# Performance work log

Measured on AMD Instinct MI355X. Metric: run time of the kernel, lower is better.

Reference implementation:

```python
import jax, jax.numpy as jnp
import numpy as np

BS, C_IN, SEQ_LEN = 16, 321, 720
PRED_LEN, PATCH_LEN, STRIDE = 720, 24, 24
N_LAYERS, D_MODEL, N_HEADS, D_FF = 3, 128, 16, 256
SEQ_PN = (SEQ_LEN - PATCH_LEN) // STRIDE + 1   # 30
PRED_PN = (PRED_LEN + PATCH_LEN - 1) // PATCH_LEN  # 30
EPS = 1e-5


def layernorm(x, g, b):
    mu = x.mean(-1, keepdims=True)
    var = x.var(-1, keepdims=True)
    return (x - mu) * jax.lax.rsqrt(var + EPS) * g + b


def setup_inputs() -> dict:
    key = jax.random.key(0)
    ks = iter(jax.random.split(key, 32))
    w = lambda shape, s=0.02: jax.random.normal(next(ks), shape, jnp.float32) * s
    L = N_LAYERS
    return {
        "z": jax.random.normal(next(ks), (BS, C_IN, SEQ_LEN), jnp.float32),
        "W_P_w": w((D_MODEL, PATCH_LEN)), "W_P_b": jnp.zeros((D_MODEL,), jnp.float32),
        "PE": 0.04 * jax.random.uniform(next(ks), (SEQ_PN, D_MODEL), jnp.float32) - 0.02,
        "dummies": 0.5 * jax.random.normal(next(ks), (C_IN, PRED_PN, PATCH_LEN), jnp.float32),
        "Wq": w((L, D_MODEL, D_MODEL)), "bq": jnp.zeros((L, D_MODEL), jnp.float32),
        "Wk": w((L, D_MODEL, D_MODEL)), "bk": jnp.zeros((L, D_MODEL), jnp.float32),
        "Wv": w((L, D_MODEL, D_MODEL)), "bv": jnp.zeros((L, D_MODEL), jnp.float32),
        "Wo": w((L, D_MODEL, D_MODEL)), "bo": jnp.zeros((L, D_MODEL), jnp.float32),
        "g1": jnp.ones((L, D_MODEL), jnp.float32), "be1": jnp.zeros((L, D_MODEL), jnp.float32),
        "W1": w((L, D_FF, D_MODEL)), "b1": jnp.zeros((L, D_FF), jnp.float32),
        "W2": w((L, D_MODEL, D_FF // 2)), "b2": jnp.zeros((L, D_MODEL), jnp.float32),
        "g2": jnp.ones((L, D_MODEL), jnp.float32), "be2": jnp.zeros((L, D_MODEL), jnp.float32),
        "proj_w": w((PATCH_LEN, D_MODEL)), "proj_b": jnp.zeros((PATCH_LEN,), jnp.float32),
    }


def reference(z, W_P_w, W_P_b, PE, dummies, Wq, bq, Wk, bk, Wv, bv, Wo, bo,
              g1, be1, W1, b1, W2, b2, g2, be2, proj_w, proj_b):
    bs, c, _ = z.shape
    d_h = D_MODEL // N_HEADS
    scale = d_h ** -0.5
    # instance norm over time (unbiased=False var)
    mean = z.mean(2, keepdims=True)
    std = jnp.sqrt(z.var(2, keepdims=True) + EPS)
    zn = (z - mean) / std
    # unfold into patches: [bs, c, S, patch_len]
    idx = jnp.arange(SEQ_PN)[:, None] * STRIDE + jnp.arange(PATCH_LEN)[None, :]
    patches = zn[:, :, idx]
    x = jnp.einsum('bcsp,dp->bcsd', patches, W_P_w) + W_P_b + PE
    x = x.reshape(bs * c, SEQ_PN, D_MODEL)                       # seq tokens
    dum = jnp.einsum('cnp,dp->cnd', dummies, W_P_w) + W_P_b      # [c, Pn, d]
    pred = jnp.broadcast_to(dum[None], (bs, c, PRED_PN, D_MODEL)).reshape(bs * c, PRED_PN, D_MODEL)
    B = bs * c
    scores = None
    for i in range(N_LAYERS):
        q = (jnp.einsum('bpd,ed->bpe', pred, Wq[i]) + bq[i]).reshape(B, PRED_PN, N_HEADS, d_h)
        k = (jnp.einsum('bsd,ed->bse', x, Wk[i]) + bk[i]).reshape(B, SEQ_PN, N_HEADS, d_h)
        v = (jnp.einsum('bsd,ed->bse', x, Wv[i]) + bv[i]).reshape(B, SEQ_PN, N_HEADS, d_h)
        s = jnp.einsum('bphd,bshd->bphs', q, k) * scale
        if scores is not None:
            s = s + scores   # residual attention scores across layers
        scores = s
        attn = jax.nn.softmax(s, axis=-1)
        o = jnp.einsum('bphs,bshd->bphd', attn, v).reshape(B, PRED_PN, D_MODEL)
        o = jnp.einsum('bpd,ed->bpe', o, Wo[i]) + bo[i]
        pred = layernorm(pred + o, g1[i], be1[i])
        h = jnp.einsum('bpd,fd->bpf', pred, W1[i]) + b1[i]
        a, gate = jnp.split(h, 2, axis=-1)
        f = jnp.einsum('bpf,df->bpd', a * jax.nn.gelu(gate, approximate=False), W2[i]) + b2[i]
        pred = layernorm(pred + f, g2[i], be2[i])
    out = pred.reshape(bs, c, PRED_PN, D_MODEL)
    out = jnp.einsum('bcnd,pd->bcnp', out, proj_w) + proj_b
    out = out.reshape(bs, c, PRED_PN * PATCH_LEN)
    return out * std[:, :, 0:1] + mean[:, :, 0:1]
```

## Files before the change

kernel.cpp:

```cpp
#include <hip/hip_runtime.h>
#include <math.h>


typedef unsigned short u16;
typedef __attribute__((ext_vector_type(8))) short short8;
typedef __attribute__((ext_vector_type(4))) float floatx4;

#define ATTN_SCALE 0.35355339059327373f
#define SB 136
#define BUFSZ (30*SB)

#define MFMA_BF16 __builtin_amdgcn_mfma_f32_16x16x32_bf16

__device__ __forceinline__ u16 f2bf(float f){
  union{ __bf16 b; u16 u; } v; v.b = (__bf16)f;
  return v.u;
}
__device__ __forceinline__ float bf2f(u16 h){
  union{unsigned u; float f;} v; v.u = ((unsigned)h)<<16;
  return v.f;
}
__device__ __forceinline__ unsigned pk2bf(float lo, float hi){
  union{ __bf16 b[2]; unsigned u; } v;
  v.b[0] = (__bf16)lo; v.b[1] = (__bf16)hi;
  return v.u;
}
__device__ __forceinline__ float dot2bf(unsigned a, unsigned b, float c){
  float d;
  asm("v_dot2_f32_bf16 %0, %1, %2, %3" : "=v"(d) : "v"(a), "v"(b), "v"(c));
  return d;
}
__device__ __forceinline__ float gelu_f(float x){
  float u = x*(1.f + 0.044715f*x*x);
  float e = __expf(-1.5957691216057308f*u);
  return x/(1.f+e);
}

__device__ __forceinline__ short8 cvt8(const float* ap){
  floatx4 f0 = *(const floatx4*)ap;
  floatx4 f1 = *(const floatx4*)(ap+4);
  short8 a;
  a[0]=(short)f2bf(f0[0]); a[1]=(short)f2bf(f0[1]);
  a[2]=(short)f2bf(f0[2]); a[3]=(short)f2bf(f0[3]);
  a[4]=(short)f2bf(f1[0]); a[5]=(short)f2bf(f1[1]);
  a[6]=(short)f2bf(f1[2]); a[7]=(short)f2bf(f1[3]);
  return a;
}
__device__ __forceinline__ short8 loadB(const u16* p){ return *(const short8*)p; }
__device__ __forceinline__ short8 loadB(const float* p){ return cvt8(p); }

__device__ __forceinline__ void epi(u16* out, floatx4 acc, float bv, float oscale,
                                    int rt, int qd, int col){
  #pragma unroll
  for (int r=0;r<4;++r){
    const int row = rt*16+qd*4+r;
    if (row<30) out[row*SB+col] = f2bf((acc[r]+bv)*oscale);
  }
}

template<typename WT>
__device__ __forceinline__ void gemm2(const u16* A, const WT* __restrict__ W,
                                      const float* __restrict__ bias, u16* out,
                                      int wave, int lane, float oscale){
  const int m=lane&15, qd=lane>>4, c0=wave*16+m;
  floatx4 acc[2][2] = {{{0.f,0.f,0.f,0.f},{0.f,0.f,0.f,0.f}},
                       {{0.f,0.f,0.f,0.f},{0.f,0.f,0.f,0.f}}};
  #pragma unroll
  for (int kt=0;kt<4;++kt){
    short8 b0 = loadB(W + c0*128       + kt*32 + qd*8);
    short8 b1 = loadB(W + (c0+64)*128  + kt*32 + qd*8);
    #pragma unroll
    for (int rt=0;rt<2;++rt){
      short8 a = *(const short8*)(A + (rt*16+m)*SB + kt*32 + qd*8);
      acc[0][rt] = MFMA_BF16(a, b0, acc[0][rt], 0,0,0);
      acc[1][rt] = MFMA_BF16(a, b1, acc[1][rt], 0,0,0);
    }
  }
  #pragma unroll
  for (int ct=0;ct<2;++ct){
    const int col = c0 + ct*64;
    const float bv = bias[col];
    #pragma unroll
    for (int rt=0;rt<2;++rt) epi(out, acc[ct][rt], bv, oscale, rt, qd, col);
  }
}

template<typename WT>
__device__ __forceinline__ void gemm_kv(const u16* A,
                                        const WT* __restrict__ Wk, const float* __restrict__ bk,
                                        const WT* __restrict__ Wv, const float* __restrict__ bv_,
                                        u16* outk, u16* outv, int wave, int lane){
  const int m=lane&15, qd=lane>>4, c0=wave*16+m;
  floatx4 acck[2][2] = {{{0.f,0.f,0.f,0.f},{0.f,0.f,0.f,0.f}},
                        {{0.f,0.f,0.f,0.f},{0.f,0.f,0.f,0.f}}};
  floatx4 accv[2][2] = {{{0.f,0.f,0.f,0.f},{0.f,0.f,0.f,0.f}},
                        {{0.f,0.f,0.f,0.f},{0.f,0.f,0.f,0.f}}};
  #pragma unroll
  for (int kt=0;kt<4;++kt){
    short8 bk0 = loadB(Wk + c0*128      + kt*32 + qd*8);
    short8 bk1 = loadB(Wk + (c0+64)*128 + kt*32 + qd*8);
    short8 bv0 = loadB(Wv + c0*128      + kt*32 + qd*8);
    short8 bv1 = loadB(Wv + (c0+64)*128 + kt*32 + qd*8);
    #pragma unroll
    for (int rt=0;rt<2;++rt){
      short8 a = *(const short8*)(A + (rt*16+m)*SB + kt*32 + qd*8);
      acck[0][rt] = MFMA_BF16(a, bk0, acck[0][rt], 0,0,0);
      acck[1][rt] = MFMA_BF16(a, bk1, acck[1][rt], 0,0,0);
      accv[0][rt] = MFMA_BF16(a, bv0, accv[0][rt], 0,0,0);
      accv[1][rt] = MFMA_BF16(a, bv1, accv[1][rt], 0,0,0);
    }
  }
  #pragma unroll
  for (int ct=0;ct<2;++ct){
    const int col = c0 + ct*64;
    const float bkb = bk[col], bvb = bv_[col];
    #pragma unroll
    for (int rt=0;rt<2;++rt){
      epi(outk, acck[ct][rt], bkb, 1.f, rt, qd, col);
      epi(outv, accv[ct][rt], bvb, 1.f, rt, qd, col);
    }
  }
}

template<typename WT>
__device__ __forceinline__ void gemm_h(const u16* A, const WT* __restrict__ W1,
                                       const float* __restrict__ b1, u16* out,
                                       int wave, int lane){
  const int m=lane&15, qd=lane>>4, c0=wave*16+m;
  floatx4 acca[2][2] = {{{0.f,0.f,0.f,0.f},{0.f,0.f,0.f,0.f}},
                        {{0.f,0.f,0.f,0.f},{0.f,0.f,0.f,0.f}}};
  floatx4 accg[2][2] = {{{0.f,0.f,0.f,0.f},{0.f,0.f,0.f,0.f}},
                        {{0.f,0.f,0.f,0.f},{0.f,0.f,0.f,0.f}}};
  #pragma unroll
  for (int kt=0;kt<4;++kt){
    short8 ba0 = loadB(W1 + c0*128        + kt*32 + qd*8);
    short8 ba1 = loadB(W1 + (c0+64)*128   + kt*32 + qd*8);
    short8 bg0 = loadB(W1 + (c0+128)*128  + kt*32 + qd*8);
    short8 bg1 = loadB(W1 + (c0+192)*128  + kt*32 + qd*8);
    #pragma unroll
    for (int rt=0;rt<2;++rt){
      short8 a = *(const short8*)(A + (rt*16+m)*SB + kt*32 + qd*8);
      acca[0][rt] = MFMA_BF16(a, ba0, acca[0][rt], 0,0,0);
      acca[1][rt] = MFMA_BF16(a, ba1, acca[1][rt], 0,0,0);
      accg[0][rt] = MFMA_BF16(a, bg0, accg[0][rt], 0,0,0);
      accg[1][rt] = MFMA_BF16(a, bg1, accg[1][rt], 0,0,0);
    }
  }
  #pragma unroll
  for (int ct=0;ct<2;++ct){
    const int ca = c0 + ct*64;
    const float bab = b1[ca], bgb = b1[128+ca];
    #pragma unroll
    for (int rt=0;rt<2;++rt){
      #pragma unroll
      for (int r=0;r<4;++r){
        const int row = rt*16+qd*4+r;
        if (row<30){
          float a = acca[ct][rt][r]+bab;
          float g = accg[ct][rt][r]+bgb;
          out[row*SB+ca] = f2bf(a * gelu_f(g));
        }
      }
    }
  }
}

__device__ __forceinline__ void ln_res_reg(float (&p0)[8], float (&p1)[8],
                                           const u16* add, u16* predb,
                                           const float* __restrict__ g, const float* __restrict__ be,
                                           int wave, int lane){
  #pragma unroll
  for (int idx=0; idx<8; ++idx){
    const int row = wave + idx*4;
    if (row < 30){
      float v0 = p0[idx] + bf2f(add[row*SB+lane]);
      float v1 = p1[idx] + bf2f(add[row*SB+lane+64]);
      float s = v0+v1, s2 = v0*v0+v1*v1;
      #pragma unroll
      for (int off=32; off>0; off>>=1){ s += __shfl_xor(s,off,64); s2 += __shfl_xor(s2,off,64); }
      float m = s*(1.f/128.f);
      float var = s2*(1.f/128.f) - m*m;
      float rstd = rsqrtf(var + 1e-5f);
      float o0 = (v0-m)*rstd*g[lane]    + be[lane];
      float o1 = (v1-m)*rstd*g[lane+64] + be[lane+64];
      p0[idx] = o0; p1[idx] = o1;
      predb[row*SB+lane]    = f2bf(o0);
      predb[row*SB+lane+64] = f2bf(o1);
    }
  }
}

__global__ void cvtw(const float* __restrict__ Wq, const float* __restrict__ Wk,
                     const float* __restrict__ Wv, const float* __restrict__ Wo,
                     const float* __restrict__ W1, const float* __restrict__ W2,
                     u16* __restrict__ ws){
  const int i = blockIdx.x*256 + threadIdx.x;
  float v;
  if      (i < 49152)  v = Wq[i];
  else if (i < 98304)  v = Wk[i-49152];
  else if (i < 147456) v = Wv[i-98304];
  else if (i < 196608) v = Wo[i-147456];
  else if (i < 294912) v = W1[i-196608];
  else                 v = W2[i-294912];
  ws[i] = f2bf(v);
}

template<typename WT>
__global__ void
__attribute__((amdgpu_flat_work_group_size(256,256), amdgpu_waves_per_eu(2)))
ts_fused(
  const float* __restrict__ z,    const float* __restrict__ WPw, const float* __restrict__ WPb,
  const float* __restrict__ PE,   const float* __restrict__ dums,
  const WT*    __restrict__ Wq_a, const float* __restrict__ bq_a,
  const WT*    __restrict__ Wk_a, const float* __restrict__ bk_a,
  const WT*    __restrict__ Wv_a, const float* __restrict__ bv_a,
  const WT*    __restrict__ Wo_a, const float* __restrict__ bo_a,
  const float* __restrict__ g1_a, const float* __restrict__ be1_a,
  const WT*    __restrict__ W1_a, const float* __restrict__ b1_a,
  const WT*    __restrict__ W2_a, const float* __restrict__ b2_a,
  const float* __restrict__ g2_a, const float* __restrict__ be2_a,
  const float* __restrict__ PJw,  const float* __restrict__ PJb,
  float* __restrict__ dout)
{
  __shared__ __align__(16) u16 SH[5*BUFSZ + 2*SB];
  __shared__ float redA[4], redB[4], stats[2];

  u16* const x_s   = SH;
  u16* const predb = SH + BUFSZ;
  u16* const bufA  = SH + 2*BUFSZ;
  u16* const bufB  = SH + 3*BUFSZ;
  u16* const bufC  = SH + 4*BUFSZ;

  const int tid  = threadIdx.x;
  const int wave = tid >> 6;
  const int lane = tid & 63;
  const int bi   = blockIdx.x;
  const int c    = bi % 321;
  const float* zr = z + bi*720;

  float s=0.f, s2=0.f;
  for (int i=tid;i<720;i+=256){ float v=zr[i]; s+=v; s2+=v*v; }
  #pragma unroll
  for (int off=32; off>0; off>>=1){ s += __shfl_xor(s,off,64); s2 += __shfl_xor(s2,off,64); }
  if (lane==0){ redA[wave]=s; redB[wave]=s2; }
  __syncthreads();
  if (tid==0){
    float S=0.f,S2=0.f;
    #pragma unroll
    for (int w=0;w<4;++w){S+=redA[w];S2+=redB[w];}
    float mu = S*(1.f/720.f);
    float var = S2*(1.f/720.f) - mu*mu;
    stats[0]=mu; stats[1]=sqrtf(var+1e-5f);
  }
  __syncthreads();
  const float mu = stats[0], sd = stats[1], rsd = 1.f/sd;

  for (int i=tid;i<720;i+=256) bufC[i] = f2bf((zr[i]-mu)*rsd);
  __syncthreads();

  {
    float* pf = (float*)(SH + 2*BUFSZ);
    const int m = lane&15, qd = lane>>4;
    const short8 z8 = {0,0,0,0,0,0,0,0};
    #pragma unroll
    for (int ct=0;ct<2;++ct){
      const int col = ct*64 + wave*16 + m;
      short8 b = (qd<3) ? cvt8(WPw + col*24 + qd*8) : z8;
      const float bv = WPb[col];
      #pragma unroll
      for (int rt=0;rt<2;++rt){
        const int pm = rt*16+m;
        short8 ax = (pm<30 && qd<3) ? *(const short8*)(bufC + pm*24 + qd*8) : z8;
        short8 ap = (pm<30 && qd<3) ? cvt8(dums + c*720 + pm*24 + qd*8) : z8;
        floatx4 accx={0.f,0.f,0.f,0.f}, accp={0.f,0.f,0.f,0.f};
        accx = MFMA_BF16(ax,b,accx,0,0,0);
        accp = MFMA_BF16(ap,b,accp,0,0,0);
        #pragma unroll
        for (int r=0;r<4;++r){
          const int row = rt*16+qd*4+r;
          if (row<30){
            float pv = accp[r]+bv;
            x_s[row*SB+col]   = f2bf(accx[r]+bv+PE[row*128+col]);
            pf[row*128+col]   = pv;
            predb[row*SB+col] = f2bf(pv);
          }
        }
      }
    }
  }
  __syncthreads();

  float p0[8], p1[8];
  {
    const float* pf = (const float*)(SH + 2*BUFSZ);
    #pragma unroll
    for (int idx=0; idx<8; ++idx){
      const int row = wave + idx*4;
      p0[idx] = (row<30) ? pf[row*128+lane]    : 0.f;
      p1[idx] = (row<30) ? pf[row*128+lane+64] : 0.f;
    }
  }
  __syncthreads();

  float sc[2][30];
  #pragma unroll
  for (int s2i=0;s2i<2;++s2i)
    #pragma unroll
    for (int i=0;i<30;++i) sc[s2i][i]=0.f;
  const int h = wave*2 + (lane>>5);
  const int p = lane & 31;

  for (int li=0; li<3; ++li){
    const WT* Wq = Wq_a + li*16384; const float* bq = bq_a + li*128;
    const WT* Wk = Wk_a + li*16384; const float* bk = bk_a + li*128;
    const WT* Wv = Wv_a + li*16384; const float* bv = bv_a + li*128;
    const WT* Wo = Wo_a + li*16384; const float* bo = bo_a + li*128;
    const WT* W1 = W1_a + li*32768; const float* b1 = b1_a + li*256;
    const WT* W2 = W2_a + li*16384; const float* b2 = b2_a + li*128;

    gemm2  (predb, Wq, bq, bufA, wave, lane, ATTN_SCALE);
    gemm_kv(x_s, Wk, bk, Wv, bv, bufB, bufC, wave, lane);
    __syncthreads();

    if (p < 30){
      #pragma unroll
      for (int s2i=0;s2i<2;++s2i){
        const int he = h + s2i*8;
        short8 qq = *(const short8*)(bufA + p*SB + he*8);
        const unsigned* qp = (const unsigned*)&qq;
        #pragma unroll
        for (int si=0; si<30; ++si){
          short8 kk = *(const short8*)(bufB + si*SB + he*8);
          const unsigned* kp = (const unsigned*)&kk;
          sc[s2i][si] = dot2bf(qp[0],kp[0],
                        dot2bf(qp[1],kp[1],
                        dot2bf(qp[2],kp[2],
                        dot2bf(qp[3],kp[3], sc[s2i][si]))));
        }
        float mx = sc[s2i][0];
        #pragma unroll
        for (int si=1; si<30; ++si) mx = fmaxf(mx, sc[s2i][si]);
        float ssum = 0.f;
        float ov[8] = {0.f,0.f,0.f,0.f,0.f,0.f,0.f,0.f};
        #pragma unroll
        for (int si=0; si<30; ++si){
          float e = __expf(sc[s2i][si]-mx);
          ssum += e;
          short8 vv = *(const short8*)(bufC + si*SB + he*8);
          #pragma unroll
          for (int j=0;j<8;++j) ov[j] += e*bf2f((u16)vv[j]);
        }
        const float rn = 1.f/ssum;
        unsigned* ob32 = (unsigned*)(bufA + p*SB + he*8);
        #pragma unroll
        for (int jj=0;jj<4;++jj)
          ob32[jj] = pk2bf(ov[2*jj]*rn, ov[2*jj+1]*rn);
      }
    }
    __syncthreads();

    gemm2(bufA, Wo, bo, bufB, wave, lane, 1.f);
    __syncthreads();
    ln_res_reg(p0, p1, bufB, predb, g1_a+li*128, be1_a+li*128, wave, lane);
    __syncthreads();

    gemm_h(predb, W1, b1, bufC, wave, lane);
    __syncthreads();
    gemm2(bufC, W2, b2, bufB, wave, lane, 1.f);
    __syncthreads();
    ln_res_reg(p0, p1, bufB, predb, g2_a+li*128, be2_a+li*128, wave, lane);
    __syncthreads();
  }

  {
    const int m = lane&15, qd = lane>>4;
    const short8 z8 = {0,0,0,0,0,0,0,0};
    const int rt = wave>>1, ct = wave&1;
    const int col = ct*16+m;
    float* orow = dout + bi*720;
    floatx4 acc = {0.f,0.f,0.f,0.f};
    #pragma unroll
    for (int kt=0;kt<4;++kt){
      const int k0 = kt*32+qd*8;
      short8 a = *(const short8*)(predb + (rt*16+m)*SB + k0);
      short8 b = (col<24) ? cvt8(PJw + col*128 + k0) : z8;
      acc = MFMA_BF16(a,b,acc,0,0,0);
    }
    if (col<24){
      const float pb = PJb[col];
      #pragma unroll
      for (int r=0;r<4;++r){
        const int row = rt*16+qd*4+r;
        if (row<30) orow[row*24+col] = (acc[r]+pb)*sd + mu;
      }
    }
  }
}

extern "C" void kernel_launch(void* const* d_in, const int* in_sizes, int n_in,
                              void* d_out, int out_size, void* d_ws, size_t ws_size,
                              hipStream_t stream) {
  (void)in_sizes; (void)n_in; (void)out_size;
  const float* z    = (const float*)d_in[0];
  const float* WPw  = (const float*)d_in[1];
  const float* WPb  = (const float*)d_in[2];
  const float* PE   = (const float*)d_in[3];
  const float* dums = (const float*)d_in[4];
  const float* Wq   = (const float*)d_in[5];
  const float* bq   = (const float*)d_in[6];
  const float* Wk   = (const float*)d_in[7];
  const float* bk   = (const float*)d_in[8];
  const float* Wv   = (const float*)d_in[9];
  const float* bv   = (const float*)d_in[10];
  const float* Wo   = (const float*)d_in[11];
  const float* bo   = (const float*)d_in[12];
  const float* g1   = (const float*)d_in[13];
  const float* be1  = (const float*)d_in[14];
  const float* W1   = (const float*)d_in[15];
  const float* b1   = (const float*)d_in[16];
  const float* W2   = (const float*)d_in[17];
  const float* b2   = (const float*)d_in[18];
  const float* g2   = (const float*)d_in[19];
  const float* be2  = (const float*)d_in[20];
  const float* PJw  = (const float*)d_in[21];
  const float* PJb  = (const float*)d_in[22];
  float* dout = (float*)d_out;

  const size_t need = (size_t)344064 * sizeof(u16);
  if (ws_size >= need){
    u16* ws = (u16*)d_ws;
    cvtw<<<dim3(1344), dim3(256), 0, stream>>>(Wq, Wk, Wv, Wo, W1, W2, ws);
    ts_fused<u16><<<dim3(5136), dim3(256), 0, stream>>>(
      z, WPw, WPb, PE, dums,
      ws,        bq, ws+49152,  bk, ws+98304, bv, ws+147456, bo,
      g1, be1, ws+196608, b1, ws+294912, b2, g2, be2, PJw, PJb, dout);
  } else {
    ts_fused<float><<<dim3(5136), dim3(256), 0, stream>>>(
      z, WPw, WPb, PE, dums,
      Wq, bq, Wk, bk, Wv, bv, Wo, bo,
      g1, be1, W1, b1, W2, b2, g2, be2, PJw, PJb, dout);
  }
}
```

Measured before the change: 864.0 us.

## Precompute K/V for all layers upfront into dedicated LDS buffers

K and V depend only on the fixed patch embedding x, so all three layers' K/V projections now run together before the layer loop. Each result goes into its own shared-memory buffer, and each layer then does only the Q projection before attention. This front-loads independent GEMM work and removes the K/V GEMM from each layer's critical path. The cost is LDS use rising from 5 to 9 buffers (about 74KB), which may cut the number of resident blocks per CU.

```diff
diff --git a/kernel.cpp b/kernel.cpp
--- a/kernel.cpp
+++ b/kernel.cpp
@@ -222,14 +222,12 @@
   const float* __restrict__ PJw,  const float* __restrict__ PJb,
   float* __restrict__ dout)
 {
-  __shared__ __align__(16) u16 SH[5*BUFSZ + 2*SB];
+  __shared__ __align__(16) u16 SH[9*BUFSZ + 2*SB];
   __shared__ float redA[4], redB[4], stats[2];
 
-  u16* const x_s   = SH;
-  u16* const predb = SH + BUFSZ;
-  u16* const bufA  = SH + 2*BUFSZ;
-  u16* const bufB  = SH + 3*BUFSZ;
-  u16* const bufC  = SH + 4*BUFSZ;
+  u16* const predb = SH;
+  u16* const bufA  = SH + BUFSZ;
+  u16* const bufB  = SH + 2*BUFSZ;
 
   const int tid  = threadIdx.x;
   const int wave = tid >> 6;
@@ -255,11 +253,11 @@
   __syncthreads();
   const float mu = stats[0], sd = stats[1], rsd = 1.f/sd;
 
-  for (int i=tid;i<720;i+=256) bufC[i] = f2bf((zr[i]-mu)*rsd);
+  for (int i=tid;i<720;i+=256) bufA[i] = f2bf((zr[i]-mu)*rsd);
   __syncthreads();
 
   {
-    float* pf = (float*)(SH + 2*BUFSZ);
+    float* pf = (float*)(SH + 3*BUFSZ);
     const int m = lane&15, qd = lane>>4;
     const short8 z8 = {0,0,0,0,0,0,0,0};
     #pragma unroll
@@ -270,7 +268,7 @@
       #pragma unroll
       for (int rt=0;rt<2;++rt){
         const int pm = rt*16+m;
-        short8 ax = (pm<30 && qd<3) ? *(const short8*)(bufC + pm*24 + qd*8) : z8;
+        short8 ax = (pm<30 && qd<3) ? *(const short8*)(bufA + pm*24 + qd*8) : z8;
         short8 ap = (pm<30 && qd<3) ? cvt8(dums + c*720 + pm*24 + qd*8) : z8;
         floatx4 accx={0.f,0.f,0.f,0.f}, accp={0.f,0.f,0.f,0.f};
         accx = MFMA_BF16(ax,b,accx,0,0,0);
@@ -280,7 +278,7 @@
           const int row = rt*16+qd*4+r;
           if (row<30){
             float pv = accp[r]+bv;
-            x_s[row*SB+col]   = f2bf(accx[r]+bv+PE[row*128+col]);
+            bufB[row*SB+col]  = f2bf(accx[r]+bv+PE[row*128+col]);
             pf[row*128+col]   = pv;
             predb[row*SB+col] = f2bf(pv);
           }
@@ -292,7 +290,7 @@
 
   float p0[8], p1[8];
   {
-    const float* pf = (const float*)(SH + 2*BUFSZ);
+    const float* pf = (const float*)(SH + 3*BUFSZ);
     #pragma unroll
     for (int idx=0; idx<8; ++idx){
       const int row = wave + idx*4;
@@ -310,16 +308,23 @@
   const int h = wave*2 + (lane>>5);
   const int p = lane & 31;
 
+  #pragma unroll
+  for (int li=0; li<3; ++li){
+    gemm_kv(bufB, Wk_a + li*16384, bk_a + li*128,
+            Wv_a + li*16384, bv_a + li*128,
+            SH + (3+2*li)*BUFSZ, SH + (4+2*li)*BUFSZ, wave, lane);
+  }
+  __syncthreads();
+
   for (int li=0; li<3; ++li){
     const WT* Wq = Wq_a + li*16384; const float* bq = bq_a + li*128;
-    const WT* Wk = Wk_a + li*16384; const float* bk = bk_a + li*128;
-    const WT* Wv = Wv_a + li*16384; const float* bv = bv_a + li*128;
     const WT* Wo = Wo_a + li*16384; const float* bo = bo_a + li*128;
     const WT* W1 = W1_a + li*32768; const float* b1 = b1_a + li*256;
     const WT* W2 = W2_a + li*16384; const float* b2 = b2_a + li*128;
-
-    gemm2  (predb, Wq, bq, bufA, wave, lane, ATTN_SCALE);
-    gemm_kv(x_s, Wk, bk, Wv, bv, bufB, bufC, wave, lane);
+    const u16* kb = SH + (3+2*li)*BUFSZ;
+    const u16* vb = SH + (4+2*li)*BUFSZ;
+
+    gemm2(predb, Wq, bq, bufA, wave, lane, ATTN_SCALE);
     __syncthreads();
 
     if (p < 30){
@@ -330,7 +335,7 @@
         const unsigned* qp = (const unsigned*)&qq;
         #pragma unroll
         for (int si=0; si<30; ++si){
-          short8 kk = *(const short8*)(bufB + si*SB + he*8);
+          short8 kk = *(const short8*)(kb + si*SB + he*8);
           const unsigned* kp = (const unsigned*)&kk;
           sc[s2i][si] = dot2bf(qp[0],kp[0],
                         dot2bf(qp[1],kp[1],
@@ -346,7 +351,7 @@
         for (int si=0; si<30; ++si){
           float e = __expf(sc[s2i][si]-mx);
           ssum += e;
-          short8 vv = *(const short8*)(bufC + si*SB + he*8);
+          short8 vv = *(const short8*)(vb + si*SB + he*8);
           #pragma unroll
           for (int j=0;j<8;++j) ov[j] += e*bf2f((u16)vv[j]);
         }
@@ -364,9 +369,9 @@
     ln_res_reg(p0, p1, bufB, predb, g1_a+li*128, be1_a+li*128, wave, lane);
     __syncthreads();
 
-    gemm_h(predb, W1, b1, bufC, wave, lane);
-    __syncthreads();
-    gemm2(bufC, W2, b2, bufB, wave, lane, 1.f);
+    gemm_h(predb, W1, b1, bufA, wave, lane);
+    __syncthreads();
+    gemm2(bufA, W2, b2, bufB, wave, lane, 1.f);
     __syncthreads();
     ln_res_reg(p0, p1, bufB, predb, g2_a+li*128, be2_a+li*128, wave, lane);
     __syncthreads();
```

Result: no change. 856.9 us (-0.8%).
